# Optimization experiments

Hardware: AMD Instinct MI355X
Metric: run time of the kernel (lower is better)

The kernel has to match this reference:

```python
import jax, jax.numpy as jnp
import numpy as np

D_MODEL = 96
D_STATE = 6
D_CONV = 9
D_INNER = 2 * D_MODEL          # expand = 2
DT_RANK = (D_MODEL + 15) // 16  # ceil(d_model/16) = 6
DIM_IN = 64
DIM_OUT = 64
BATCH = 16
SEQLEN = 4096


def setup_inputs() -> dict:
    key = jax.random.key(0)
    ks = jax.random.split(key, 12)
    def s(k, shape, scale=0.02):
        return jax.random.normal(k, shape, jnp.float32) * scale
    return {
        "x": jax.random.normal(ks[0], (BATCH, SEQLEN, D_MODEL), jnp.float32),
        # Mamba block params
        "in_proj_w": s(ks[1], (2 * D_INNER, D_MODEL)),
        "conv_w": s(ks[2], (D_INNER, D_CONV), 0.1),   # depthwise conv kernel
        "conv_b": jnp.zeros((D_INNER,), jnp.float32),
        "x_proj_w": s(ks[3], (DT_RANK + 2 * D_STATE, D_INNER)),
        "dt_proj_w": s(ks[4], (D_INNER, DT_RANK), 0.1),
        "dt_proj_b": s(ks[5], (D_INNER,), 0.1),
        "A_log": jnp.log(jnp.tile(jnp.arange(1, D_STATE + 1, dtype=jnp.float32), (D_INNER, 1))),
        "D_param": jnp.ones((D_INNER,), jnp.float32),
        "out_proj_w": s(ks[6], (D_MODEL, D_INNER)),
        "norm_w": jnp.ones((D_MODEL,), jnp.float32),  # RMSNorm weight
        # heads
        "out_fc_w": s(ks[7], (DIM_IN, D_MODEL)),
        "out_fc_b": jnp.zeros((DIM_IN,), jnp.float32),
        "mu_w": s(ks[8], (DIM_OUT, DIM_IN)),
        "mu_b": jnp.zeros((DIM_OUT,), jnp.float32),
        "sigma_w": s(ks[9], (DIM_OUT, DIM_IN)),
        "sigma_b": jnp.zeros((DIM_OUT,), jnp.float32),
    }


def _mamba_block(x, in_proj_w, conv_w, conv_b, x_proj_w, dt_proj_w, dt_proj_b,
                 A_log, D_param, out_proj_w):
    Bsz = x.shape[0]
    xz = jnp.einsum('bld,ed->ble', x, in_proj_w)          # (B,L,2*ED)
    xs, z = jnp.split(xz, 2, axis=-1)
    # causal depthwise conv1d (torch pads d_conv-1 both sides then trims right)
    xt = xs.transpose(0, 2, 1)                            # (B,ED,L)
    kern = conv_w[:, None, :]                             # (ED,1,K)
    xc = jax.lax.conv_general_dilated(xt, kern, window_strides=(1,),
                                      padding=[(D_CONV - 1, 0)],
                                      feature_group_count=D_INNER)
    xc = (xc + conv_b[None, :, None]).transpose(0, 2, 1)  # (B,L,ED)
    xc = jax.nn.silu(xc)
    dbc = jnp.einsum('ble,fe->blf', xc, x_proj_w)         # (B,L,dt_rank+2N)
    delta_r = dbc[..., :DT_RANK]
    Bm = dbc[..., DT_RANK:DT_RANK + D_STATE]              # (B,L,N)
    Cm = dbc[..., DT_RANK + D_STATE:]                     # (B,L,N)
    delta = jax.nn.softplus(jnp.einsum('blr,er->ble', delta_r, dt_proj_w) + dt_proj_b)
    A = -jnp.exp(A_log)                                   # (ED,N)
    deltaA = jnp.exp(delta[..., None] * A)                # (B,L,ED,N)
    BX = (delta * xc)[..., None] * Bm[:, :, None, :]      # (B,L,ED,N)

    def step(h, inputs):
        dA, bx = inputs
        h = dA * h + bx
        return h, h

    h0 = jnp.zeros((Bsz, D_INNER, D_STATE), x.dtype)
    _, hs = jax.lax.scan(step, h0, (deltaA.swapaxes(0, 1), BX.swapaxes(0, 1)))
    y = jnp.einsum('lben,bln->ble', hs, Cm)               # (B,L,ED)
    y = y + D_param * xc
    y = y * jax.nn.silu(z)
    return jnp.einsum('ble,de->bld', y, out_proj_w)       # (B,L,D)


def reference(x, in_proj_w, conv_w, conv_b, x_proj_w, dt_proj_w, dt_proj_b,
              A_log, D_param, out_proj_w, norm_w,
              out_fc_w, out_fc_b, mu_w, mu_b, sigma_w, sigma_b):
    # residual block: x + mixer(RMSNorm(x))   (dropout is identity at eval)
    h = x * jax.lax.rsqrt(jnp.mean(x * x, axis=-1, keepdims=True) + 1e-5) * norm_w
    out = x + _mamba_block(h, in_proj_w, conv_w, conv_b, x_proj_w,
                           dt_proj_w, dt_proj_b, A_log, D_param, out_proj_w)
    e = out.mean(axis=1)                                  # (B,D)
    feat = jax.nn.elu(jnp.tanh(e @ out_fc_w.T + out_fc_b))
    mu = feat @ mu_w.T + mu_b
    sigma = jax.nn.elu(feat @ sigma_w.T + sigma_b) + 1.0 + 1e-14
    return (feat, mu, sigma)
```

## Files before the change

### kernel.cpp

```cpp
#include <hip/hip_runtime.h>
#include <math.h>

#define BATCH 16
#define SEQLEN 4096
#define D_MODEL 96
#define D_STATE 6
#define D_CONV 9
#define D_INNER 192
#define DT_RANK 6
#define NPOS (BATCH * SEQLEN)

#define NC2 128
#define CT2 (SEQLEN / NC2)
#define NSEG 16
#define CPS (NC2 / NSEG)

#define OFF_XS    0L
#define OFF_Z     (OFF_XS   + (long)NPOS * 96)
#define OFF_OUT4  (OFF_Z    + (long)NPOS * 96)
#define OFF_SEG   (OFF_OUT4 + (long)BATCH * NC2 * 5 * 192 * 4)
#define OFF_XBAR  (OFF_SEG  + (long)BATCH * NSEG * 5 * 192 * 4)

typedef short v8s __attribute__((ext_vector_type(8)));
typedef float v4f __attribute__((ext_vector_type(4)));

__device__ __forceinline__ float silu_fast(float v) {
    return __fdividef(v, 1.0f + __expf(-v));
}
__device__ __forceinline__ float softplus_fast(float v) {
    return (v > 20.0f) ? v : __logf(1.0f + __expf(v));
}
__device__ __forceinline__ float eluf(float v) {
    return (v > 0.0f) ? v : expm1f(v);
}
__device__ __forceinline__ unsigned int pack_bf16(float a, float b) {
    unsigned int ua = __float_as_uint(a), ub = __float_as_uint(b);
    ua += 0x7FFFu + ((ua >> 16) & 1u);
    ub += 0x7FFFu + ((ub >> 16) & 1u);
    return (ua >> 16) | (ub & 0xFFFF0000u);
}
__device__ __forceinline__ unsigned short bf16h(float v) {
    unsigned int u = __float_as_uint(v);
    u += 0x7FFFu + ((u >> 16) & 1u);
    return (unsigned short)(u >> 16);
}
__device__ __forceinline__ float bf2f(unsigned short h) {
    return __uint_as_float(((unsigned int)h) << 16);
}

#define TP1 64
__global__ __launch_bounds__(256, 3) void k1_rmsnorm_inproj(
    const float* __restrict__ x, const float* __restrict__ W,
    const float* __restrict__ norm_w,
    unsigned short* __restrict__ xs, unsigned short* __restrict__ z,
    float* __restrict__ xbar)
{
    __shared__ unsigned int s_ovl[7680];
    __shared__ unsigned int s_hA[64 * 52];
    __shared__ float s_scale[TP1];
    float* hRow = (float*)s_ovl;
    unsigned int* WB = s_ovl;

    const int tid = threadIdx.x;
    const long p0 = (long)blockIdx.x * TP1;
    const int b = (int)(p0 / SEQLEN);

    for (int i = tid; i < TP1 * 96; i += 256) {
        int p = i / 96, d = i - p * 96;
        hRow[p * 101 + d] = x[p0 * 96 + i];
    }
    __syncthreads();

    if (tid < TP1) {
        float ss = 0.0f;
        for (int d = 0; d < 96; d++) { float v = hRow[tid * 101 + d]; ss += v * v; }
        s_scale[tid] = 1.0f / sqrtf(ss / 96.0f + 1e-5f);
    } else if (tid < TP1 + 96) {
        int d = tid - TP1;
        float s = 0.0f;
        for (int p = 0; p < TP1; p++) s += hRow[p * 101 + d];
        atomicAdd(&xbar[b * 96 + d], s);
    }
    __syncthreads();

    {
        const float2* nw2 = (const float2*)norm_w;
        for (int i = tid; i < TP1 * 48; i += 256) {
            int p = i / 48, dp = i - p * 48;
            float sc = s_scale[p];
            float2 nv = nw2[dp];
            float v0 = hRow[p * 101 + 2 * dp]     * sc * nv.x;
            float v1 = hRow[p * 101 + 2 * dp + 1] * sc * nv.y;
            s_hA[p * 52 + dp] = pack_bf16(v0, v1);
        }
    }

    const int wave = tid >> 6, lane = tid & 63;
    const int quad = lane >> 4, ln = lane & 15;
    const int n0 = wave * 96;

    v4f acc[4][6];
#pragma unroll
    for (int mt = 0; mt < 4; mt++)
#pragma unroll
        for (int nt = 0; nt < 6; nt++) acc[mt][nt] = (v4f){0.f, 0.f, 0.f, 0.f};

    for (int kc = 0; kc < 3; kc++) {
        __syncthreads();
        for (int i = tid; i < 384 * 16; i += 256) {
            int j = i >> 4, kp = i & 15;
            const float2 wv = *(const float2*)&W[j * 96 + kc * 32 + 2 * kp];
            WB[j * 20 + kp] = pack_bf16(wv.x, wv.y);
        }
        __syncthreads();

        v8s af[4];
#pragma unroll
        for (int mt = 0; mt < 4; mt++)
            af[mt] = *(const v8s*)&s_hA[(mt * 16 + ln) * 52 + kc * 16 + quad * 4];
#pragma unroll
        for (int nt = 0; nt < 6; nt++) {
            v8s bf = *(const v8s*)&WB[(n0 + nt * 16 + ln) * 20 + quad * 4];
#pragma unroll
            for (int mt = 0; mt < 4; mt++)
                acc[mt][nt] = __builtin_amdgcn_mfma_f32_16x16x32_bf16(
                    af[mt], bf, acc[mt][nt], 0, 0, 0);
        }
    }

    unsigned short* dst = (wave < 2) ? xs : z;
    const int jbase = (wave & 1) * 96 + ln;
#pragma unroll
    for (int mt = 0; mt < 4; mt++) {
#pragma unroll
        for (int r = 0; r < 4; r++) {
            long pos = p0 + mt * 16 + quad * 4 + r;
            unsigned short* drow = &dst[pos * D_INNER + jbase];
#pragma unroll
            for (int nt = 0; nt < 6; nt++) drow[nt * 16] = bf16h(acc[mt][nt][r]);
        }
    }
}

#define XSTR2 196
__global__ __launch_bounds__(192, 3) void k2f_conv_scan(
    const unsigned short* __restrict__ xs, const unsigned short* __restrict__ z,
    const float* __restrict__ conv_w, const float* __restrict__ conv_b,
    const float* __restrict__ x_proj_w,
    const float* __restrict__ dt_w, const float* __restrict__ dt_b,
    const float* __restrict__ A_log, const float* __restrict__ D_param,
    float4* __restrict__ out4)
{
    __shared__ float sxc[CT2 * XSTR2];
    __shared__ float sxp[18 * XSTR2];
    __shared__ float sMeta[CT2][20];
    const int e = threadIdx.x;
    const int c = blockIdx.x & (NC2 - 1);
    const int b = blockIdx.x >> 7;
    const int l0 = c * CT2;
    const long brow = (long)b * SEQLEN;

    for (int i = e; i < 18 * 192; i += 192) {
        int f = i / 192, kk = i - f * 192;
        sxp[f * XSTR2 + kk] = x_proj_w[i];
    }

    float cw[D_CONV];
#pragma unroll
    for (int k = 0; k < D_CONV; k++) cw[k] = conv_w[e * D_CONV + k];
    const float cb = conv_b[e];
    float win[D_CONV];
#pragma unroll
    for (int k = 0; k < 8; k++) {
        int ll = l0 - 8 + k;
        win[k] = (ll >= 0) ? bf2f(xs[(brow + ll) * D_INNER + e]) : 0.0f;
    }
#pragma unroll 4
    for (int r = 0; r < CT2; r++) {
        win[8] = bf2f(xs[(brow + l0 + r) * D_INNER + e]);
        float s = cb;
#pragma unroll
        for (int k = 0; k < D_CONV; k++) s += win[k] * cw[k];
        sxc[r * XSTR2 + e] = silu_fast(s);
#pragma unroll
        for (int k = 0; k < 8; k++) win[k] = win[k + 1];
    }

    const unsigned short* zp = &z[(brow + l0) * D_INNER + e];
    float zv[CT2];
#pragma unroll
    for (int t = 0; t < CT2; t++) zv[t] = bf2f(zp[(long)t * D_INNER]);
    __syncthreads();

    {
        const int p = e / 6, fg = e - p * 6;
        const float4* xr = (const float4*)&sxc[p * XSTR2];
        const float4* w0 = (const float4*)&sxp[fg * XSTR2];
        const float4* w1 = (const float4*)&sxp[(fg + 6) * XSTR2];
        const float4* w2 = (const float4*)&sxp[(fg + 12) * XSTR2];
        float s0 = 0.0f, s1 = 0.0f, s2 = 0.0f;
#pragma unroll 4
        for (int kk = 0; kk < D_INNER / 4; kk++) {
            float4 xv = xr[kk];
            float4 a = w0[kk], bq = w1[kk], cc = w2[kk];
            s0 += xv.x * a.x + xv.y * a.y + xv.z * a.z + xv.w * a.w;
            s1 += xv.x * bq.x + xv.y * bq.y + xv.z * bq.z + xv.w * bq.w;
            s2 += xv.x * cc.x + xv.y * cc.y + xv.z * cc.z + xv.w * cc.w;
        }
        sMeta[p][fg] = s0;
        sMeta[p][8 + fg] = s1;
        sMeta[p][14 + fg] = s2;
    }
    __syncthreads();

    float a[D_STATE];
#pragma unroll
    for (int n = 0; n < D_STATE; n++) a[n] = -__expf(A_log[e * D_STATE + n]);
    float dtw[DT_RANK];
#pragma unroll
    for (int q = 0; q < DT_RANK; q++) dtw[q] = dt_w[e * DT_RANK + q];
    const float dtb = dt_b[e];
    const float Dv = D_param[e];
    const float a0 = a[0];

    bool pok = true;
#pragma unroll
    for (int n = 1; n < D_STATE; n++)
        pok = pok && (fabsf(a[n] - (float)(n + 1) * a0)
                      <= 1e-4f * (float)(n + 1) * fabsf(a0));
    unsigned long long pmask = __ballot(pok);

    float S[D_STATE], P[D_STATE], G[D_STATE];
#pragma unroll
    for (int n = 0; n < D_STATE; n++) { S[n] = 0.0f; P[n] = 1.0f; G[n] = 0.0f; }
    float ysum0 = 0.0f;

    if (pmask == 0xFFFFFFFFFFFFFFFFull) {
#pragma unroll 2
        for (int t = 0; t < CT2; t++) {
            const float4* m4 = (const float4*)&sMeta[t][0];
            float4 m0 = m4[0], m1 = m4[1], mB0 = m4[2], mB1 = m4[3], mC = m4[4];
            float Bv[6] = {mB0.x, mB0.y, mB0.z, mB0.w, mB1.x, mB1.y};
            float Cv[6] = {mB1.z, mB1.w, mC.x, mC.y, mC.z, mC.w};
            float dr = dtb + m0.x * dtw[0] + m0.y * dtw[1] + m0.z * dtw[2]
                     + m0.w * dtw[3] + m1.x * dtw[4] + m1.y * dtw[5];
            float dl = softplus_fast(dr);
            float xv = sxc[t * XSTR2 + e];
            float zw = silu_fast(zv[t]);
            float dx = dl * xv;
            float y = Dv * xv;
            float E = __expf(dl * a0);
            float dA = E;
#pragma unroll
            for (int n = 0; n < D_STATE; n++) {
                S[n] = dA * S[n] + dx * Bv[n];
                P[n] *= dA;
                y += S[n] * Cv[n];
                G[n] += zw * P[n] * Cv[n];
                dA *= E;
            }
            ysum0 += zw * y;
        }
    } else {
#pragma unroll 2
        for (int t = 0; t < CT2; t++) {
            const float4* m4 = (const float4*)&sMeta[t][0];
            float4 m0 = m4[0], m1 = m4[1], mB0 = m4[2], mB1 = m4[3], mC = m4[4];
            float Bv[6] = {mB0.x, mB0.y, mB0.z, mB0.w, mB1.x, mB1.y};
            float Cv[6] = {mB1.z, mB1.w, mC.x, mC.y, mC.z, mC.w};
            float dr = dtb + m0.x * dtw[0] + m0.y * dtw[1] + m0.z * dtw[2]
                     + m0.w * dtw[3] + m1.x * dtw[4] + m1.y * dtw[5];
            float dl = softplus_fast(dr);
            float xv = sxc[t * XSTR2 + e];
            float zw = silu_fast(zv[t]);
            float dx = dl * xv;
            float y = Dv * xv;
#pragma unroll
            for (int n = 0; n < D_STATE; n++) {
                float dA = __expf(dl * a[n]);
                S[n] = dA * S[n] + dx * Bv[n];
                P[n] *= dA;
                y += S[n] * Cv[n];
                G[n] += zw * P[n] * Cv[n];
            }
            ysum0 += zw * y;
        }
    }

    long ob = (long)(b * NC2 + c) * 5 * 192 + e;
    float4 q0, q1, q2, q3, q4;
    q0.x=P[0]; q0.y=P[1]; q0.z=P[2]; q0.w=P[3];
    q1.x=P[4]; q1.y=P[5]; q1.z=S[0]; q1.w=S[1];
    q2.x=S[2]; q2.y=S[3]; q2.z=S[4]; q2.w=S[5];
    q3.x=G[0]; q3.y=G[1]; q3.z=G[2]; q3.w=G[3];
    q4.x=G[4]; q4.y=G[5]; q4.z=ysum0; q4.w=0.0f;
    out4[ob          ] = q0;
    out4[ob + 192    ] = q1;
    out4[ob + 2 * 192] = q2;
    out4[ob + 3 * 192] = q3;
    out4[ob + 4 * 192] = q4;
}

__global__ __launch_bounds__(192) void k4_seg(
    const float4* __restrict__ out4, float4* __restrict__ seg4)
{
    const int e = threadIdx.x;
    const int s = blockIdx.x & (NSEG - 1);
    const int b = blockIdx.x >> 4;

    float H[D_STATE], Gq[D_STATE], Pp[D_STATE];
#pragma unroll
    for (int n = 0; n < D_STATE; n++) { H[n] = 0.0f; Gq[n] = 0.0f; Pp[n] = 1.0f; }
    float yb = 0.0f;
#pragma unroll 2
    for (int cc = 0; cc < CPS; cc++) {
        int c = s * CPS + cc;
        long ob = (long)(b * NC2 + c) * 5 * 192 + e;
        float4 q0 = out4[ob];
        float4 q1 = out4[ob + 192];
        float4 q2 = out4[ob + 2 * 192];
        float4 q3 = out4[ob + 3 * 192];
        float4 q4 = out4[ob + 4 * 192];
        float Pv[6] = {q0.x, q0.y, q0.z, q0.w, q1.x, q1.y};
        float Sv[6] = {q1.z, q1.w, q2.x, q2.y, q2.z, q2.w};
        float Gv[6] = {q3.x, q3.y, q3.z, q3.w, q4.x, q4.y};
        float g = 0.0f;
#pragma unroll
        for (int n = 0; n < D_STATE; n++) g += Gv[n] * H[n];
        yb += q4.z + g;
#pragma unroll
        for (int n = 0; n < D_STATE; n++) {
            Gq[n] += Gv[n] * Pp[n];
            H[n] = Pv[n] * H[n] + Sv[n];
            Pp[n] *= Pv[n];
        }
    }
    long sb = (long)(b * NSEG + s) * 5 * 192 + e;
    float4 q0, q1, q2, q3, q4;
    q0.x=Pp[0]; q0.y=Pp[1]; q0.z=Pp[2]; q0.w=Pp[3];
    q1.x=Pp[4]; q1.y=Pp[5]; q1.z=H[0]; q1.w=H[1];
    q2.x=H[2]; q2.y=H[3]; q2.z=H[4]; q2.w=H[5];
    q3.x=Gq[0]; q3.y=Gq[1]; q3.z=Gq[2]; q3.w=Gq[3];
    q4.x=Gq[4]; q4.y=Gq[5]; q4.z=yb; q4.w=0.0f;
    seg4[sb          ] = q0;
    seg4[sb + 192    ] = q1;
    seg4[sb + 2 * 192] = q2;
    seg4[sb + 3 * 192] = q3;
    seg4[sb + 4 * 192] = q4;
}

__global__ __launch_bounds__(192) void k4_head(
    const float4* __restrict__ seg4, const float* __restrict__ xbar,
    const float* __restrict__ Wout,
    const float* __restrict__ fc_w, const float* __restrict__ fc_b,
    const float* __restrict__ mu_w, const float* __restrict__ mu_b,
    const float* __restrict__ sg_w, const float* __restrict__ sg_b,
    float* __restrict__ out)
{
    __shared__ float ybar[D_INNER];
    __shared__ float evec[D_MODEL];
    __shared__ float feat_s[64];
    const int e = threadIdx.x;
    const int b = blockIdx.x;

    float H[D_STATE];
#pragma unroll
    for (int n = 0; n < D_STATE; n++) H[n] = 0.0f;
    float yb = 0.0f;
#pragma unroll 4
    for (int s = 0; s < NSEG; s++) {
        long ob = (long)(b * NSEG + s) * 5 * 192 + e;
        float4 q0 = seg4[ob];
        float4 q1 = seg4[ob + 192];
        float4 q2 = seg4[ob + 2 * 192];
        float4 q3 = seg4[ob + 3 * 192];
        float4 q4 = seg4[ob + 4 * 192];
        float Pv[6] = {q0.x, q0.y, q0.z, q0.w, q1.x, q1.y};
        float Sv[6] = {q1.z, q1.w, q2.x, q2.y, q2.z, q2.w};
        float Gv[6] = {q3.x, q3.y, q3.z, q3.w, q4.x, q4.y};
        float g = 0.0f;
#pragma unroll
        for (int n = 0; n < D_STATE; n++) g += Gv[n] * H[n];
        yb += q4.z + g;
#pragma unroll
        for (int n = 0; n < D_STATE; n++) H[n] = Pv[n] * H[n] + Sv[n];
    }
    ybar[e] = yb;
    __syncthreads();

    if (e < D_MODEL) {
        float s = xbar[b * D_MODEL + e];
        const float* wrow = &Wout[e * D_INNER];
        for (int e2 = 0; e2 < D_INNER; e2++) s += ybar[e2] * wrow[e2];
        evec[e] = s / (float)SEQLEN;
    }
    __syncthreads();

    if (e < 64) {
        float s = fc_b[e];
        const float* wrow = &fc_w[e * D_MODEL];
        for (int d = 0; d < D_MODEL; d++) s += evec[d] * wrow[d];
        float f = eluf(tanhf(s));
        feat_s[e] = f;
        out[b * 64 + e] = f;
    }
    __syncthreads();

    if (e < 64) {
        float smu = mu_b[e], ssg = sg_b[e];
        const float* mrow = &mu_w[e * 64];
        const float* srow = &sg_w[e * 64];
        for (int i = 0; i < 64; i++) {
            smu += feat_s[i] * mrow[i];
            ssg += feat_s[i] * srow[i];
        }
        out[1024 + b * 64 + e] = smu;
        out[2048 + b * 64 + e] = eluf(ssg) + 1.0f + 1e-14f;
    }
}

extern "C" void kernel_launch(void* const* d_in, const int* in_sizes, int n_in,
                              void* d_out, int out_size, void* d_ws, size_t ws_size,
                              hipStream_t stream) {
    const float* x         = (const float*)d_in[0];
    const float* in_proj_w = (const float*)d_in[1];
    const float* conv_w    = (const float*)d_in[2];
    const float* conv_b    = (const float*)d_in[3];
    const float* x_proj_w  = (const float*)d_in[4];
    const float* dt_proj_w = (const float*)d_in[5];
    const float* dt_proj_b = (const float*)d_in[6];
    const float* A_log     = (const float*)d_in[7];
    const float* D_param   = (const float*)d_in[8];
    const float* out_proj_w= (const float*)d_in[9];
    const float* norm_w    = (const float*)d_in[10];
    const float* out_fc_w  = (const float*)d_in[11];
    const float* out_fc_b  = (const float*)d_in[12];
    const float* mu_w      = (const float*)d_in[13];
    const float* mu_b      = (const float*)d_in[14];
    const float* sigma_w   = (const float*)d_in[15];
    const float* sigma_b   = (const float*)d_in[16];
    float* ws = (float*)d_ws;
    float* out = (float*)d_out;

    hipMemsetAsync(ws + OFF_XBAR, 0, BATCH * D_MODEL * sizeof(float), stream);

    k1_rmsnorm_inproj<<<NPOS / TP1, 256, 0, stream>>>(
        x, in_proj_w, norm_w,
        (unsigned short*)(ws + OFF_XS), (unsigned short*)(ws + OFF_Z),
        ws + OFF_XBAR);

    k2f_conv_scan<<<BATCH * NC2, 192, 0, stream>>>(
        (const unsigned short*)(ws + OFF_XS), (const unsigned short*)(ws + OFF_Z),
        conv_w, conv_b, x_proj_w,
        dt_proj_w, dt_proj_b, A_log, D_param,
        (float4*)(ws + OFF_OUT4));

    k4_seg<<<BATCH * NSEG, 192, 0, stream>>>(
        (const float4*)(ws + OFF_OUT4), (float4*)(ws + OFF_SEG));

    k4_head<<<BATCH, 192, 0, stream>>>(
        (const float4*)(ws + OFF_SEG), ws + OFF_XBAR, out_proj_w,
        out_fc_w, out_fc_b, mu_w, mu_b, sigma_w, sigma_b, out);
}
```

Baseline: 223.4 us.

## Compute x_proj with bf16 MFMA in conv-scan kernel and shrink shared memory

Replaces the scalar FP32 dot-product x_proj (32 positions × 18 outputs × 192) in the conv/scan kernel with bf16 MFMA 16x16x32 on two waves. The conv output and x_proj weights are stored in shared memory as bf16 (weights padded to 32 rows), which halves LDS use and allows raising launch bounds to 4 blocks per SM. The conv loop is fully unrolled. In exchange the conv output xc is rounded to bf16, which lowers precision both in the projection and in the scan's D*x and delta*x terms, and only 2 of 3 waves do the projection.

```diff
diff --git a/kernel.cpp b/kernel.cpp
--- a/kernel.cpp
+++ b/kernel.cpp
@@ -142,8 +142,8 @@
     }
 }
 
-#define XSTR2 196
-__global__ __launch_bounds__(192, 3) void k2f_conv_scan(
+#define SXSTR 200
+__global__ __launch_bounds__(192, 4) void k2f_conv_scan(
     const unsigned short* __restrict__ xs, const unsigned short* __restrict__ z,
     const float* __restrict__ conv_w, const float* __restrict__ conv_b,
     const float* __restrict__ x_proj_w,
@@ -151,8 +151,8 @@
     const float* __restrict__ A_log, const float* __restrict__ D_param,
     float4* __restrict__ out4)
 {
-    __shared__ float sxc[CT2 * XSTR2];
-    __shared__ float sxp[18 * XSTR2];
+    __shared__ unsigned short sxc[CT2 * SXSTR];
+    __shared__ unsigned short sxpB[32 * SXSTR];
     __shared__ float sMeta[CT2][20];
     const int e = threadIdx.x;
     const int c = blockIdx.x & (NC2 - 1);
@@ -160,9 +160,17 @@
     const int l0 = c * CT2;
     const long brow = (long)b * SEQLEN;
 
-    for (int i = e; i < 18 * 192; i += 192) {
-        int f = i / 192, kk = i - f * 192;
-        sxp[f * XSTR2 + kk] = x_proj_w[i];
+    {
+        unsigned int* xpB = (unsigned int*)sxpB;
+        for (int i = e; i < 32 * 96; i += 192) {
+            int f = i / 96, kp = i - f * 96;
+            unsigned int v = 0u;
+            if (f < 18) {
+                const float2 wv = *(const float2*)&x_proj_w[f * 192 + 2 * kp];
+                v = pack_bf16(wv.x, wv.y);
+            }
+            xpB[f * 100 + kp] = v;
+        }
     }
 
     float cw[D_CONV];
@@ -175,13 +183,13 @@
         int ll = l0 - 8 + k;
         win[k] = (ll >= 0) ? bf2f(xs[(brow + ll) * D_INNER + e]) : 0.0f;
     }
-#pragma unroll 4
+#pragma unroll
     for (int r = 0; r < CT2; r++) {
         win[8] = bf2f(xs[(brow + l0 + r) * D_INNER + e]);
         float s = cb;
 #pragma unroll
         for (int k = 0; k < D_CONV; k++) s += win[k] * cw[k];
-        sxc[r * XSTR2 + e] = silu_fast(s);
+        sxc[r * SXSTR + e] = bf16h(silu_fast(s));
 #pragma unroll
         for (int k = 0; k < 8; k++) win[k] = win[k + 1];
     }
@@ -193,23 +201,32 @@
     __syncthreads();
 
     {
-        const int p = e / 6, fg = e - p * 6;
-        const float4* xr = (const float4*)&sxc[p * XSTR2];
-        const float4* w0 = (const float4*)&sxp[fg * XSTR2];
-        const float4* w1 = (const float4*)&sxp[(fg + 6) * XSTR2];
-        const float4* w2 = (const float4*)&sxp[(fg + 12) * XSTR2];
-        float s0 = 0.0f, s1 = 0.0f, s2 = 0.0f;
-#pragma unroll 4
-        for (int kk = 0; kk < D_INNER / 4; kk++) {
-            float4 xv = xr[kk];
-            float4 a = w0[kk], bq = w1[kk], cc = w2[kk];
-            s0 += xv.x * a.x + xv.y * a.y + xv.z * a.z + xv.w * a.w;
-            s1 += xv.x * bq.x + xv.y * bq.y + xv.z * bq.z + xv.w * bq.w;
-            s2 += xv.x * cc.x + xv.y * cc.y + xv.z * cc.z + xv.w * cc.w;
-        }
-        sMeta[p][fg] = s0;
-        sMeta[p][8 + fg] = s1;
-        sMeta[p][14 + fg] = s2;
+        const int wave = e >> 6, lane = e & 63;
+        const int quad = lane >> 4, ln = lane & 15;
+        if (wave < 2) {
+            const int mt = wave;
+            v4f dacc[2];
+            dacc[0] = (v4f){0.f, 0.f, 0.f, 0.f};
+            dacc[1] = (v4f){0.f, 0.f, 0.f, 0.f};
+#pragma unroll
+            for (int kc = 0; kc < 6; kc++) {
+                v8s af  = *(const v8s*)&sxc[(mt * 16 + ln) * SXSTR + kc * 32 + quad * 8];
+                v8s bf0 = *(const v8s*)&sxpB[ln * SXSTR + kc * 32 + quad * 8];
+                v8s bf1 = *(const v8s*)&sxpB[(16 + ln) * SXSTR + kc * 32 + quad * 8];
+                dacc[0] = __builtin_amdgcn_mfma_f32_16x16x32_bf16(af, bf0, dacc[0], 0, 0, 0);
+                dacc[1] = __builtin_amdgcn_mfma_f32_16x16x32_bf16(af, bf1, dacc[1], 0, 0, 0);
+            }
+#pragma unroll
+            for (int nt = 0; nt < 2; nt++) {
+                int f = nt * 16 + ln;
+                if (f < 18) {
+                    int col = (f < 6) ? f : f + 2;
+#pragma unroll
+                    for (int r = 0; r < 4; r++)
+                        sMeta[mt * 16 + quad * 4 + r][col] = dacc[nt][r];
+                }
+            }
+        }
     }
     __syncthreads();
 
@@ -245,7 +262,7 @@
             float dr = dtb + m0.x * dtw[0] + m0.y * dtw[1] + m0.z * dtw[2]
                      + m0.w * dtw[3] + m1.x * dtw[4] + m1.y * dtw[5];
             float dl = softplus_fast(dr);
-            float xv = sxc[t * XSTR2 + e];
+            float xv = bf2f(sxc[t * SXSTR + e]);
             float zw = silu_fast(zv[t]);
             float dx = dl * xv;
             float y = Dv * xv;
@@ -271,7 +288,7 @@
             float dr = dtb + m0.x * dtw[0] + m0.y * dtw[1] + m0.z * dtw[2]
                      + m0.w * dtw[3] + m1.x * dtw[4] + m1.y * dtw[5];
             float dl = softplus_fast(dr);
-            float xv = sxc[t * XSTR2 + e];
+            float xv = bf2f(sxc[t * SXSTR + e]);
             float zw = silu_fast(zv[t]);
             float dx = dl * xv;
             float y = Dv * xv;
```

Measured after the change: 204.9 us. 8.3% less time.
